# Optimization experiments

Hardware: AMD Instinct MI355X
Metric: run time of the kernel (lower is better)

The kernel has to match this reference:

```python
import jax, jax.numpy as jnp
import numpy as np

DX, DY, MR, MBAR, NT, B, GOUT = 16, 8, 64, 256, 9, 4, 64
HX, EX, HRNN, HB = 1024, 512, 512, 2048
BB_IN = 1 + EX + HRNN


def setup_inputs() -> dict:
    key = jax.random.key(0)
    ks = jax.random.split(key, 12)
    total = (NT - 1) * MBAR + 1  # 2049 hidden-process time points
    X = jax.random.randint(ks[0], (B, total, DX), 0, 50).astype(jnp.float32)  # molecule counts
    Y = jax.random.normal(ks[1], (B, NT, DY), dtype=jnp.float32)
    # R: cumulative integrated reaction rates (non-decreasing in time)
    R = jnp.cumsum(jax.random.uniform(ks[2], (B, total, MR), dtype=jnp.float32) * 0.01, axis=1)
    stoich = (jax.random.randint(ks[3], (DX, MR), 0, 3) - 1).astype(jnp.float32)  # entries in {-1,0,1}
    times_t = jnp.linspace(0.0, 8.0, NT).astype(jnp.float32)
    times_tau = jnp.linspace(0.0, 1.0, MBAR).astype(jnp.float32)
    sc = lambda k, sh: jax.random.normal(k, sh, dtype=jnp.float32) * np.float32(1.0 / np.sqrt(sh[0]))
    Wx1, bx1 = sc(ks[4], (DX, HX)), jnp.zeros(HX, jnp.float32)
    Wx2, bx2 = sc(ks[5], (HX, EX)), jnp.zeros(EX, jnp.float32)
    Wih = sc(ks[6], (DY, HRNN))
    Whh = sc(ks[7], (HRNN, HRNN))
    bh = jnp.zeros(HRNN, jnp.float32)
    Wb1, bb1 = sc(ks[8], (BB_IN, HB)), jnp.zeros(HB, jnp.float32)
    Wb2, bb2 = sc(ks[9], (HB, GOUT)), jnp.zeros(GOUT, jnp.float32)
    return dict(X=X, Y=Y, R=R, stoich=stoich, times_t=times_t, times_tau=times_tau,
                Wx1=Wx1, bx1=bx1, Wx2=Wx2, bx2=bx2, Wih=Wih, Whh=Whh, bh=bh,
                Wb1=Wb1, bb1=bb1, Wb2=Wb2, bb2=bb2, k=1, k_prime=1, q=0, q_prime=1)


def reference(X, Y, R, stoich, times_t, times_tau,
              Wx1, bx1, Wx2, bx2, Wih, Whh, bh, Wb1, bb1, Wb2, bb2,
              k, k_prime, q, q_prime):
    """stochastic_integral_vectorized: gather displaced states, run the
    martingale network forward on base and displaced states, masked
    accumulation weighted by rate increments. Returns [GOUT]."""
    m_bar = times_tau.shape[0]
    base = k_prime * m_bar

    # --- Y encoder (Elman RNN over the observation slice, final hidden state) ---
    Yslice = Y[q, k + 1:, :]                       # [T_rem, DY]
    def rnn_step(h, y):
        return jnp.tanh(y @ Wih + h @ Whh + bh), None
    eY, _ = jax.lax.scan(rnn_step, jnp.zeros(Whh.shape[0], X.dtype), Yslice)  # [HRNN]

    # --- batched martingale forward: t [N], Xb [N, DX] -> [N, GOUT] ---
    def batched_forward(t, Xb):
        eX = jnp.tanh(Xb @ Wx1 + bx1) @ Wx2 + bx2          # [N, EX]
        eYb = jnp.broadcast_to(eY, (Xb.shape[0], eY.shape[0]))
        inp = jnp.concatenate([t[:, None], eX, eYb], axis=1)  # [N, 1+EX+HRNN]
        return jnp.tanh(inp @ Wb1 + bb1) @ Wb2 + bb2       # [N, GOUT]

    Xbase = X[q_prime, base:base + m_bar, :]               # [M_bar, DX]
    t = times_t[k] + times_tau                              # [M_bar]
    nn = batched_forward(t, Xbase)                          # [M_bar, GOUT]

    mr = stoich.shape[1]
    X_disp = Xbase[None, :, :] + stoich.T[:, None, :]       # [MR, M_bar, DX]
    valid = jnp.all(X_disp >= 0, axis=-1)                   # [MR, M_bar]
    nn_disp = batched_forward(jnp.tile(t, mr),
                              X_disp.reshape(mr * m_bar, -1)).reshape(mr, m_bar, -1)

    R_delta = R[q_prime, base + 1:base + m_bar + 1, :] - R[q_prime, base:base + m_bar, :]  # [M_bar, MR]
    si = jnp.einsum('jmg,mj,jm->g', nn_disp - nn[None], R_delta, valid.astype(nn.dtype))
    return si
```

## Files before the change

kernel.cpp:

```cpp
#include <hip/hip_runtime.h>
#include <math.h>

#define DXc   16
#define MRc   64
#define MBARc 256
#define NTc   9
#define DYc   8
#define HXc   1024
#define EXc   512
#define HRc   512
#define HBc   2048
#define GOUTc 64
#define TOTc  2049

using bf16x8 = __attribute__((ext_vector_type(8))) short;
using f32x4  = __attribute__((ext_vector_type(4))) float;

typedef unsigned int u32;
typedef u32 __attribute__((address_space(1))) gbl_u32;
typedef u32 __attribute__((address_space(3))) lds_u32;

__device__ __forceinline__ float fast_tanh(float x){
    float e = __expf(2.0f * x);
    return 1.0f - 2.0f / (e + 1.0f);
}

__device__ __forceinline__ short f2bf(float f){
    unsigned u = __builtin_bit_cast(unsigned, f);
    u = (u + 0x7FFFu + ((u >> 16) & 1u)) >> 16;
    return (short)u;
}

__device__ __forceinline__ void gld_lds16(const short* g, short* l){
    __builtin_amdgcn_global_load_lds((const gbl_u32*)g, (lds_u32*)l, 16, 0, 0);
}

__global__ void prep_kernel(const float* __restrict__ stoich, const float* __restrict__ Wx1,
                            const float* __restrict__ Wx2, const float* __restrict__ Wb1,
                            const float* __restrict__ X, const float* __restrict__ R,
                            const float* __restrict__ bx1, const float* __restrict__ bx2,
                            const int* kpptr, const int* qpptr,
                            float* __restrict__ SW, short* __restrict__ Wx2a,
                            short* __restrict__ Wb1p, float* __restrict__ XW,
                            float* __restrict__ T1, float* __restrict__ wrow,
                            float* __restrict__ hb0, float* __restrict__ dacc,
                            float* __restrict__ outz, float* __restrict__ eXb,
                            int* __restrict__ cnt){
    int b = blockIdx.x, tid = threadIdx.x;
    if (b < 256){
        int idx = b * 256 + tid;
        int j = idx >> 10, c = idx & 1023;
        float acc = 0.f;
        #pragma unroll
        for (int d = 0; d < DXc; ++d) acc += stoich[d * MRc + j] * Wx1[d * HXc + c];
        SW[idx] = acc;
    } else if (b < 512){
        size_t grp = (size_t)(b - 256) * 256 + tid;
        int lane = grp & 63;
        size_t t2 = grp >> 6;
        int kt = t2 & 15, mt = t2 >> 4;
        int c  = mt * 16 + (lane & 15);
        int e0 = kt * 32 + ((lane >> 4) << 3);
        short o8[8];
        #pragma unroll
        for (int jj = 0; jj < 8; ++jj) o8[jj] = f2bf(Wx2[(size_t)c * EXc + e0 + jj]);
        *(bf16x8*)(Wx2a + grp * 8) = *(bf16x8*)o8;
    } else if (b < 1024){
        size_t grp = (size_t)(b - 512) * 256 + tid;
        int lane = grp & 63;
        size_t t2 = grp >> 6;
        int kt = t2 & 15, nt = t2 >> 4;
        int n  = nt * 16 + (lane & 15);
        int k0 = kt * 32 + ((lane >> 4) << 3);
        short o8[8];
        #pragma unroll
        for (int jj = 0; jj < 8; ++jj) o8[jj] = f2bf(Wb1[(size_t)(1 + k0 + jj) * HBc + n]);
        *(bf16x8*)(Wb1p + grp * 8) = *(bf16x8*)o8;
    } else if (b < 2048){
        int idx = (b - 1024) * 256 + tid;
        int m = idx >> 10, c = idx & 1023;
        int base = kpptr[0] * MBARc;
        const float* xr = X + ((size_t)qpptr[0] * TOTc + base + m) * DXc;
        float acc = bx1[c];
        #pragma unroll
        for (int d = 0; d < DXc; ++d) acc += xr[d] * Wx1[d * HXc + c];
        XW[idx] = acc;
        T1[idx] = fast_tanh(acc);
    } else if (b < 2112){
        int j = b - 2048, m = tid;
        int base = kpptr[0] * MBARc;
        int qp = qpptr[0];
        const float* xr = X + ((size_t)qp * TOTc + base + m) * DXc;
        bool valid = true;
        #pragma unroll
        for (int d = 0; d < DXc; ++d) valid = valid && (xr[d] + stoich[d * MRc + j] >= 0.f);
        size_t rb = (size_t)qp * TOTc * MRc;
        float rd = R[rb + (size_t)(base + 1 + m) * MRc + j] - R[rb + (size_t)(base + m) * MRc + j];
        wrow[j * MBARc + m] = valid ? rd : 0.f;
    } else if (b == 2112){
        hb0[tid] = 0.f; hb0[tid + 256] = 0.f;
        #pragma unroll
        for (int l = 0; l < 8; ++l) dacc[tid + l * 256] = 0.f;
        if (tid < GOUTc) outz[tid] = 0.f;
        if (tid < 4) cnt[tid] = 0;
    } else {
        int idx = (b - 2113) * 256 + tid;
        eXb[idx] = bx2[idx & 511];
    }
}

#define MMGRID(aa, bb) {                                                       \
    _Pragma("unroll") for (int i_ = 0; i_ < 4; ++i_)                           \
        _Pragma("unroll") for (int j_ = 0; j_ < 4; ++j_)                       \
            acc[i_][j_] = __builtin_amdgcn_mfma_f32_16x16x32_bf16(aa[i_], bb[j_], acc[i_][j_], 0, 0, 0); }

__device__ __forceinline__ void stage32(const short* __restrict__ Ap, const short* __restrict__ Bp,
                                        short* As, short* Bs,
                                        int at0, int bt0, int s, int KTOT, int wave, int lane){
    #pragma unroll
    for (int c = 0; c < 4; ++c){
        int ci = wave * 4 + c;
        int half = ci >> 3;
        int t    = ci & 7;
        const short* src = half ? (Bp + ((size_t)(bt0 + t) * KTOT + s) * 512 + lane * 8)
                                : (Ap + ((size_t)(at0 + t) * KTOT + s) * 512 + lane * 8);
        short* dst = (half ? Bs : As) + t * 512;
        gld_lds16(src, dst);
    }
}

#define STAGE_COMPUTE(As, Bs) {                                                       \
    bf16x8 af[4], bfr[4];                                                             \
    _Pragma("unroll") for (int i_ = 0; i_ < 4; ++i_)                                  \
        af[i_] = *(const bf16x8*)((As) + ((wm * 4 + i_) * 512) + lane * 8);           \
    _Pragma("unroll") for (int j_ = 0; j_ < 4; ++j_)                                  \
        bfr[j_] = *(const bf16x8*)((Bs) + ((wn * 4 + j_) * 512) + lane * 8);          \
    MMGRID(af, bfr); }

__global__ __launch_bounds__(256) void mega2_kernel(
    const float* __restrict__ Y, const float* __restrict__ Wih,
    const float* __restrict__ Whh, const float* __restrict__ bh,
    const float* __restrict__ Wb1, const float* __restrict__ bb1,
    const int* kptr, const int* qptr,
    float* __restrict__ hb0, float* __restrict__ hb1,
    int* __restrict__ cnt, float* __restrict__ cY,
    const short* __restrict__ Wx2a, const short* __restrict__ Wb1p,
    short* __restrict__ W12p,
    const float* __restrict__ Wx2, float* __restrict__ eXb,
    float* __restrict__ Z2Bacc,
    const float* __restrict__ XW, const float* __restrict__ T1,
    const float* __restrict__ SW, short* __restrict__ A1p){
    __shared__ __align__(16) char smem[34816];
    int b = blockIdx.x, tid = threadIdx.x;
    if (b < 8){
        float* hs   = (float*)smem;
        float (*psum)[64] = (float(*)[64])(smem + 2048);
        int o = tid & 63, seg = tid >> 6;
        int out = b * 64 + o;
        int k = kptr[0], q = qptr[0];
        hs[tid] = 0.f; hs[tid + 256] = 0.f;
        __syncthreads();
        for (int s = 0; s < 8; ++s){
            float* dst = (s & 1) ? hb0 : hb1;
            if (s > 0){
                const float* src = (s & 1) ? hb1 : hb0;
                if (tid == 0){
                    int guard = 0;
                    while (__hip_atomic_load(cnt, __ATOMIC_ACQUIRE, __HIP_MEMORY_SCOPE_AGENT) < 8 * s
                           && ++guard < (1 << 26)) {}
                }
                __syncthreads();
                hs[tid]       = __hip_atomic_load(src + tid,       __ATOMIC_RELAXED, __HIP_MEMORY_SCOPE_AGENT);
                hs[tid + 256] = __hip_atomic_load(src + tid + 256, __ATOMIC_RELAXED, __HIP_MEMORY_SCOPE_AGENT);
                __syncthreads();
            }
            int t = k + 1 + s;
            if (t < NTc){
                int k0 = seg * 128;
                float a0 = 0.f, a1 = 0.f, a2 = 0.f, a3 = 0.f;
                #pragma unroll 4
                for (int kk = 0; kk < 128; kk += 4){
                    a0 += hs[k0 + kk + 0] * Whh[(size_t)(k0 + kk + 0) * HRc + out];
                    a1 += hs[k0 + kk + 1] * Whh[(size_t)(k0 + kk + 1) * HRc + out];
                    a2 += hs[k0 + kk + 2] * Whh[(size_t)(k0 + kk + 2) * HRc + out];
                    a3 += hs[k0 + kk + 3] * Whh[(size_t)(k0 + kk + 3) * HRc + out];
                }
                psum[seg][o] = (a0 + a1) + (a2 + a3);
                __syncthreads();
                if (seg == 0){
                    float a = psum[0][o] + psum[1][o] + psum[2][o] + psum[3][o];
                    const float* y = Y + (q * NTc + t) * DYc;
                    float z = bh[out];
                    #pragma unroll
                    for (int d = 0; d < DYc; ++d) z += y[d] * Wih[d * HRc + out];
                    __hip_atomic_store(dst + out, fast_tanh(z + a), __ATOMIC_RELEASE, __HIP_MEMORY_SCOPE_AGENT);
                }
                __syncthreads();
            } else {
                if (seg == 0)
                    __hip_atomic_store(dst + out, hs[out], __ATOMIC_RELEASE, __HIP_MEMORY_SCOPE_AGENT);
                __syncthreads();
            }
            if (tid == 0)
                __hip_atomic_fetch_add(cnt, 1, __ATOMIC_RELEASE, __HIP_MEMORY_SCOPE_AGENT);
        }
        if (tid == 0){
            int guard = 0;
            while (__hip_atomic_load(cnt, __ATOMIC_ACQUIRE, __HIP_MEMORY_SCOPE_AGENT) < 64
                   && ++guard < (1 << 26)) {}
        }
        __syncthreads();
        hs[tid]       = __hip_atomic_load(hb0 + tid,       __ATOMIC_RELAXED, __HIP_MEMORY_SCOPE_AGENT);
        hs[tid + 256] = __hip_atomic_load(hb0 + tid + 256, __ATOMIC_RELAXED, __HIP_MEMORY_SCOPE_AGENT);
        __syncthreads();
        int h = b * 256 + tid;
        float acc = 0.f;
        #pragma unroll 4
        for (int e = 0; e < HRc; ++e)
            acc += hs[e] * Wb1[(size_t)(1 + EXc + e) * HBc + h];
        cY[h] = bb1[h] + acc;
    } else if (b < 136){
        short* As0 = (short*)smem;
        short* As1 = (short*)(smem + 8192);
        short* Bs0 = (short*)(smem + 16384);
        short* Bs1 = (short*)(smem + 24576);
        const int KTOT = 16, S = 16;
        int wave = tid >> 6, lane = tid & 63;
        int wm = wave >> 1, wn = wave & 1;
        int b2 = b - 8;
        int bx = b2 & 15, by = b2 >> 4;
        int quad = lane >> 4, llo = lane & 15;
        f32x4 acc[4][4];
        #pragma unroll
        for (int i = 0; i < 4; ++i)
            #pragma unroll
            for (int j = 0; j < 4; ++j) acc[i][j] = (f32x4){0.f, 0.f, 0.f, 0.f};
        stage32(Wx2a, Wb1p, As0, Bs0, by * 8, bx * 8, 0, KTOT, wave, lane);
        for (int s = 0; s < S; ++s){
            short* Asc = (s & 1) ? As1 : As0;
            short* Bsc = (s & 1) ? Bs1 : Bs0;
            short* Asn = (s & 1) ? As0 : As1;
            short* Bsn = (s & 1) ? Bs0 : Bs1;
            __syncthreads();
            if (s + 1 < S)
                stage32(Wx2a, Wb1p, Asn, Bsn, by * 8, bx * 8, s + 1, KTOT, wave, lane);
            STAGE_COMPUTE(Asc, Bsc);
        }
        #pragma unroll
        for (int j = 0; j < 4; ++j){
            int h = bx * 128 + wn * 64 + j * 16 + llo;
            #pragma unroll
            for (int i = 0; i < 4; ++i){
                #pragma unroll
                for (int r = 0; r < 4; ++r){
                    int c = by * 128 + wm * 64 + i * 16 + quad * 4 + r;
                    W12p[(((size_t)(h >> 4) * 32 + (c >> 5)) * 64 + ((c & 31) >> 3) * 16 + llo) * 8 + (c & 7)] =
                        f2bf(acc[i][j][r]);
                }
            }
        }
    } else if (b < 648){
        float* t1s = (float*)smem;
        int bb = b - 136;
        int mg = bb & 31, eh = (bb >> 5) & 1, kq = bb >> 6;
        int m0 = mg * 8, e = eh * 256 + tid, k0 = kq * 128;
        #pragma unroll
        for (int l = 0; l < 4; ++l){
            int idx = tid + l * 256;
            t1s[idx] = T1[(size_t)(m0 + (idx >> 7)) * HXc + k0 + (idx & 127)];
        }
        __syncthreads();
        float acc[8] = {};
        #pragma unroll 4
        for (int kk = 0; kk < 128; ++kk){
            float wv = Wx2[(size_t)(k0 + kk) * EXc + e];
            #pragma unroll
            for (int mm = 0; mm < 8; ++mm) acc[mm] += t1s[mm * 128 + kk] * wv;
        }
        #pragma unroll
        for (int mm = 0; mm < 8; ++mm)
            atomicAdd(&eXb[(size_t)(m0 + mm) * EXc + e], acc[mm]);
        __syncthreads();
        if (tid == 0)
            __hip_atomic_fetch_add(cnt + 1, 1, __ATOMIC_RELEASE, __HIP_MEMORY_SCOPE_AGENT);
    } else if (b < 8840){
        size_t grp = (size_t)(b - 648) * 256 + tid;
        int lane = grp & 63;
        size_t t2 = grp >> 6;
        int kt = t2 & 31;
        int mt = (int)(t2 >> 5);
        int m  = mt * 16 + (lane & 15);
        int c0 = kt * 32 + ((lane >> 4) << 3);
        int j    = m >> 8;
        int mloc = m & 255;
        const float* xwr = XW + (size_t)mloc * HXc + c0;
        const float* t1r = T1 + (size_t)mloc * HXc + c0;
        const float* swr = SW + (size_t)j * HXc + c0;
        short o8[8];
        #pragma unroll
        for (int i = 0; i < 8; ++i)
            o8[i] = f2bf(fast_tanh(xwr[i] + swr[i]) - t1r[i]);
        *(bf16x8*)(A1p + grp * 8) = *(bf16x8*)o8;
    } else {
        float* exs = (float*)smem;
        if (tid == 0){
            int guard = 0;
            while (__hip_atomic_load(cnt + 1, __ATOMIC_ACQUIRE, __HIP_MEMORY_SCOPE_AGENT) < 512
                   && ++guard < (1 << 26)) {}
        }
        __syncthreads();
        int bb = b - 8840;
        int mg = bb & 31, hh = (bb >> 5) & 7, kq = bb >> 8;
        int m0 = mg * 8, h = hh * 256 + tid, k0 = kq * 256;
        #pragma unroll
        for (int l = 0; l < 8; ++l){
            int idx = tid + l * 256;
            exs[idx] = __hip_atomic_load(eXb + (size_t)(m0 + (idx >> 8)) * EXc + k0 + (idx & 255),
                                         __ATOMIC_RELAXED, __HIP_MEMORY_SCOPE_AGENT);
        }
        __syncthreads();
        float acc[8] = {};
        #pragma unroll 4
        for (int kk = 0; kk < 256; ++kk){
            float wv = Wb1[(size_t)(1 + k0 + kk) * HBc + h];
            #pragma unroll
            for (int mm = 0; mm < 8; ++mm) acc[mm] += exs[mm * 256 + kk] * wv;
        }
        #pragma unroll
        for (int mm = 0; mm < 8; ++mm)
            atomicAdd(&Z2Bacc[(size_t)(m0 + mm) * HBc + h], acc[mm]);
    }
}

__device__ __forceinline__ void stage24(const short* __restrict__ Ap, const short* __restrict__ Bp,
                                        short* As, short* Bs,
                                        int at0, int bt0, int s, int wave, int lane){
    #pragma unroll
    for (int c = 0; c < 6; ++c){
        int ci = wave * 6 + c;
        const short* src;
        short* dst;
        if (ci < 8){
            src = Ap + ((size_t)(at0 + ci) * 32 + s) * 512 + lane * 8;
            dst = As + ci * 512;
        } else {
            int t = ci - 8;
            src = Bp + ((size_t)(bt0 + t) * 32 + s) * 512 + lane * 8;
            dst = Bs + t * 512;
        }
        gld_lds16(src, dst);
    }
}

__global__ __launch_bounds__(256, 2) void gemm_big(
    const short* __restrict__ Ap, const short* __restrict__ Bp,
    const float* __restrict__ Z2Bacc, const float* __restrict__ Wb1,
    const float* __restrict__ cY, const float* __restrict__ times_t,
    const float* __restrict__ times_tau, const int* kptr,
    const float* __restrict__ wrow, float* __restrict__ dacc){
    const int S = 32;
    __shared__ __align__(16) short Asb[2][4096];
    __shared__ __align__(16) short Bsb[2][8192];
    int tid = threadIdx.x;
    int wave = tid >> 6, lane = tid & 63;
    int wm = wave >> 1, wn = wave & 1;
    int bm = blockIdx.x, bn = blockIdx.y;
    int quad = lane >> 4, llo = lane & 15;
    f32x4 acc[4][8];
    #pragma unroll
    for (int i = 0; i < 4; ++i)
        #pragma unroll
        for (int j = 0; j < 8; ++j) acc[i][j] = (f32x4){0.f, 0.f, 0.f, 0.f};
    stage24(Ap, Bp, Asb[0], Bsb[0], bm * 8, bn * 16, 0, wave, lane);
    for (int s = 0; s < S; ++s){
        int buf = s & 1;
        __syncthreads();
        if (s + 1 < S)
            stage24(Ap, Bp, Asb[buf ^ 1], Bsb[buf ^ 1], bm * 8, bn * 16, s + 1, wave, lane);
        {
            bf16x8 af[4], bfr[8];
            #pragma unroll
            for (int i = 0; i < 4; ++i)
                af[i] = *(const bf16x8*)(Asb[buf] + ((wm * 4 + i) * 512) + lane * 8);
            #pragma unroll
            for (int j = 0; j < 8; ++j)
                bfr[j] = *(const bf16x8*)(Bsb[buf] + ((wn * 8 + j) * 512) + lane * 8);
            #pragma unroll
            for (int i = 0; i < 4; ++i)
                #pragma unroll
                for (int j = 0; j < 8; ++j)
                    acc[i][j] = __builtin_amdgcn_mfma_f32_16x16x32_bf16(af[i], bfr[j], acc[i][j], 0, 0, 0);
        }
    }
    float tk = times_t[kptr[0]];
    int nj[8];
    float w0n[8], cyn[8];
    #pragma unroll
    for (int j = 0; j < 8; ++j){
        nj[j]  = bn * 256 + wn * 128 + j * 16 + llo;
        w0n[j] = Wb1[nj[j]];
        cyn[j] = cY[nj[j]];
    }
    float part[8] = {};
    #pragma unroll
    for (int i = 0; i < 4; ++i){
        #pragma unroll
        for (int r = 0; r < 4; ++r){
            int m = bm * 128 + wm * 64 + i * 16 + quad * 4 + r;
            float wr = wrow[m];
            float tm = tk + times_tau[m & 255];
            const float* zrow = Z2Bacc + (size_t)(m & 255) * HBc;
            #pragma unroll
            for (int j = 0; j < 8; ++j){
                float zb  = zrow[nj[j]] + tm * w0n[j] + cyn[j];
                float tb  = fast_tanh(zb);
                float tdz = fast_tanh(acc[i][j][r]);
                float num = tdz * (1.0f - tb * tb);
                float den = 1.0f + tb * tdz;
                part[j] += wr * num * __builtin_amdgcn_rcpf(den);
            }
        }
    }
    #pragma unroll
    for (int j = 0; j < 8; ++j){
        part[j] += __shfl_xor(part[j], 16);
        part[j] += __shfl_xor(part[j], 32);
    }
    __shared__ float redn[256];
    redn[tid] = 0.f;
    __syncthreads();
    if (lane < 16){
        #pragma unroll
        for (int j = 0; j < 8; ++j)
            atomicAdd(&redn[wn * 128 + j * 16 + llo], part[j]);
    }
    __syncthreads();
    atomicAdd(&dacc[bn * 256 + tid], redn[tid]);
}

__global__ void out_kernel(const float* __restrict__ dacc, const float* __restrict__ Wb2,
                           float* __restrict__ out){
    __shared__ float red[4][64];
    int tid = threadIdx.x;
    int g = tid & 63, seg = tid >> 6;
    int h0 = blockIdx.x * 256 + seg * 64;
    float s = 0.f;
    #pragma unroll 8
    for (int hh = 0; hh < 64; ++hh)
        s += dacc[h0 + hh] * Wb2[(size_t)(h0 + hh) * GOUTc + g];
    red[seg][g] = s;
    __syncthreads();
    if (tid < 64)
        atomicAdd(&out[tid], red[0][tid] + red[1][tid] + red[2][tid] + red[3][tid]);
}

extern "C" void kernel_launch(void* const* d_in, const int* in_sizes, int n_in,
                              void* d_out, int out_size, void* d_ws, size_t ws_size,
                              hipStream_t stream){
    const float* X         = (const float*)d_in[0];
    const float* Y         = (const float*)d_in[1];
    const float* R         = (const float*)d_in[2];
    const float* stoich    = (const float*)d_in[3];
    const float* times_t   = (const float*)d_in[4];
    const float* times_tau = (const float*)d_in[5];
    const float* Wx1 = (const float*)d_in[6];
    const float* bx1 = (const float*)d_in[7];
    const float* Wx2 = (const float*)d_in[8];
    const float* bx2 = (const float*)d_in[9];
    const float* Wih = (const float*)d_in[10];
    const float* Whh = (const float*)d_in[11];
    const float* bh  = (const float*)d_in[12];
    const float* Wb1 = (const float*)d_in[13];
    const float* bb1 = (const float*)d_in[14];
    const float* Wb2 = (const float*)d_in[15];
    const int* kp  = (const int*)d_in[17];
    const int* kpp = (const int*)d_in[18];
    const int* qp  = (const int*)d_in[19];
    const int* qpp = (const int*)d_in[20];
    float* out = (float*)d_out;

    float* ws     = (float*)d_ws;
    float* hb0    = ws;
    float* hb1    = ws + 512;
    float* cY     = ws + 1024;
    float* dacc   = ws + 3072;
    float* wrow   = ws + 5120;
    float* SW     = ws + 21504;
    float* XW     = ws + 87040;
    float* T1     = ws + 349184;
    float* eXb    = ws + 611328;
    float* Z2Bacc = ws + 742400;
    short* A1p    = (short*)(ws + 1266688);
    short* Wx2a   = (short*)(ws + 9655296);
    short* Wb1p   = (short*)(ws + 9917440);
    short* W12p   = (short*)(ws + 10441728);
    int*   cnt    = (int*)(ws + 11490304);

    hipMemsetAsync(Z2Bacc, 0, (size_t)MBARc * HBc * sizeof(float), stream);
    prep_kernel  <<<2625, 256, 0, stream>>>(stoich, Wx1, Wx2, Wb1, X, R, bx1, bx2, kpp, qpp,
                                            SW, Wx2a, Wb1p, XW, T1, wrow, hb0, dacc, out,
                                            eXb, cnt);
    mega2_kernel <<<9352, 256, 0, stream>>>(Y, Wih, Whh, bh, Wb1, bb1, kp, qp, hb0, hb1, cnt, cY,
                                            Wx2a, Wb1p, W12p, Wx2, eXb, Z2Bacc, XW, T1, SW, A1p);
    gemm_big     <<<dim3(128, 8), 256, 0, stream>>>(A1p, W12p, Z2Bacc, Wb1, cY,
                                                    times_t, times_tau, kp, wrow, dacc);
    out_kernel   <<<8,    256, 0, stream>>>(dacc, Wb2, out);
}
```

Baseline: 307.3 us.

## Move RNN encoder into final GEMM kernel and tile Wb1 repack via LDS

New measurement: 789.6 us. +157.0%, slower.

```diff
diff --git a/kernel.cpp b/kernel.cpp
--- a/kernel.cpp
+++ b/kernel.cpp
@@ -35,27 +35,54 @@
     __builtin_amdgcn_global_load_lds((const gbl_u32*)g, (lds_u32*)l, 16, 0, 0);
 }
 
-__global__ void prep_kernel(const float* __restrict__ stoich, const float* __restrict__ Wx1,
-                            const float* __restrict__ Wx2, const float* __restrict__ Wb1,
-                            const float* __restrict__ X, const float* __restrict__ R,
-                            const float* __restrict__ bx1, const float* __restrict__ bx2,
-                            const int* kpptr, const int* qpptr,
-                            float* __restrict__ SW, short* __restrict__ Wx2a,
-                            short* __restrict__ Wb1p, float* __restrict__ XW,
-                            float* __restrict__ T1, float* __restrict__ wrow,
-                            float* __restrict__ hb0, float* __restrict__ dacc,
-                            float* __restrict__ outz, float* __restrict__ eXb,
-                            int* __restrict__ cnt){
+__global__ __launch_bounds__(256) void prep_kernel(
+    const float* __restrict__ stoich, const float* __restrict__ Wx1,
+    const float* __restrict__ Wx2, const float* __restrict__ Wb1,
+    const float* __restrict__ X, const float* __restrict__ R,
+    const float* __restrict__ bx1, const float* __restrict__ bx2,
+    const int* kpptr, const int* qpptr,
+    float* __restrict__ SW, short* __restrict__ Wx2a,
+    short* __restrict__ Wb1p, float* __restrict__ XW,
+    float* __restrict__ T1, float* __restrict__ wrow,
+    float* __restrict__ dacc, float* __restrict__ outz,
+    float* __restrict__ eXb, int* __restrict__ cnt){
+    __shared__ __align__(16) short wtile[32 * 514];
     int b = blockIdx.x, tid = threadIdx.x;
-    if (b < 256){
-        int idx = b * 256 + tid;
+    if (b < 16){
+        int kt = b;
+        int krow0 = 1 + kt * 32;
+        for (int chunk = 0; chunk < 4; ++chunk){
+            int c0 = chunk * 512;
+            #pragma unroll
+            for (int l = 0; l < 64; ++l){
+                int idx = tid + l * 256;
+                int r = idx >> 9, c = idx & 511;
+                wtile[r * 514 + c] = f2bf(Wb1[(size_t)(krow0 + r) * HBc + c0 + c]);
+            }
+            __syncthreads();
+            #pragma unroll
+            for (int v = 0; v < 8; ++v){
+                int vecid = tid + v * 256;
+                int ntl = vecid >> 6, lane = vecid & 63;
+                int nl = ntl * 16 + (lane & 15);
+                int kl = (lane >> 4) * 8;
+                short o8[8];
+                #pragma unroll
+                for (int jj = 0; jj < 8; ++jj) o8[jj] = wtile[(kl + jj) * 514 + nl];
+                int nt = chunk * 32 + ntl;
+                *(bf16x8*)(Wb1p + (((size_t)nt * 16 + kt) * 64 + lane) * 8) = *(bf16x8*)o8;
+            }
+            __syncthreads();
+        }
+    } else if (b < 272){
+        int idx = (b - 16) * 256 + tid;
         int j = idx >> 10, c = idx & 1023;
         float acc = 0.f;
         #pragma unroll
         for (int d = 0; d < DXc; ++d) acc += stoich[d * MRc + j] * Wx1[d * HXc + c];
         SW[idx] = acc;
-    } else if (b < 512){
-        size_t grp = (size_t)(b - 256) * 256 + tid;
+    } else if (b < 528){
+        size_t grp = (size_t)(b - 272) * 256 + tid;
         int lane = grp & 63;
         size_t t2 = grp >> 6;
         int kt = t2 & 15, mt = t2 >> 4;
@@ -65,19 +92,8 @@
         #pragma unroll
         for (int jj = 0; jj < 8; ++jj) o8[jj] = f2bf(Wx2[(size_t)c * EXc + e0 + jj]);
         *(bf16x8*)(Wx2a + grp * 8) = *(bf16x8*)o8;
-    } else if (b < 1024){
-        size_t grp = (size_t)(b - 512) * 256 + tid;
-        int lane = grp & 63;
-        size_t t2 = grp >> 6;
-        int kt = t2 & 15, nt = t2 >> 4;
-        int n  = nt * 16 + (lane & 15);
-        int k0 = kt * 32 + ((lane >> 4) << 3);
-        short o8[8];
-        #pragma unroll
-        for (int jj = 0; jj < 8; ++jj) o8[jj] = f2bf(Wb1[(size_t)(1 + k0 + jj) * HBc + n]);
-        *(bf16x8*)(Wb1p + grp * 8) = *(bf16x8*)o8;
-    } else if (b < 2048){
-        int idx = (b - 1024) * 256 + tid;
+    } else if (b < 1552){
+        int idx = (b - 528) * 256 + tid;
         int m = idx >> 10, c = idx & 1023;
         int base = kpptr[0] * MBARc;
         const float* xr = X + ((size_t)qpptr[0] * TOTc + base + m) * DXc;
@@ -86,8 +102,8 @@
         for (int d = 0; d < DXc; ++d) acc += xr[d] * Wx1[d * HXc + c];
         XW[idx] = acc;
         T1[idx] = fast_tanh(acc);
-    } else if (b < 2112){
-        int j = b - 2048, m = tid;
+    } else if (b < 1616){
+        int j = b - 1552, m = tid;
         int base = kpptr[0] * MBARc;
         int qp = qpptr[0];
         const float* xr = X + ((size_t)qp * TOTc + base + m) * DXc;
@@ -97,14 +113,13 @@
         size_t rb = (size_t)qp * TOTc * MRc;
         float rd = R[rb + (size_t)(base + 1 + m) * MRc + j] - R[rb + (size_t)(base + m) * MRc + j];
         wrow[j * MBARc + m] = valid ? rd : 0.f;
-    } else if (b == 2112){
-        hb0[tid] = 0.f; hb0[tid + 256] = 0.f;
+    } else if (b == 1616){
         #pragma unroll
         for (int l = 0; l < 8; ++l) dacc[tid + l * 256] = 0.f;
         if (tid < GOUTc) outz[tid] = 0.f;
         if (tid < 4) cnt[tid] = 0;
     } else {
-        int idx = (b - 2113) * 256 + tid;
+        int idx = (b - 1617) * 256 + tid;
         eXb[idx] = bx2[idx & 511];
     }
 }
@@ -137,24 +152,167 @@
         bfr[j_] = *(const bf16x8*)((Bs) + ((wn * 4 + j_) * 512) + lane * 8);          \
     MMGRID(af, bfr); }
 
-__global__ __launch_bounds__(256) void mega2_kernel(
-    const float* __restrict__ Y, const float* __restrict__ Wih,
-    const float* __restrict__ Whh, const float* __restrict__ bh,
-    const float* __restrict__ Wb1, const float* __restrict__ bb1,
-    const int* kptr, const int* qptr,
-    float* __restrict__ hb0, float* __restrict__ hb1,
-    int* __restrict__ cnt, float* __restrict__ cY,
+__global__ __launch_bounds__(256) void mega_kernel(
     const short* __restrict__ Wx2a, const short* __restrict__ Wb1p,
     short* __restrict__ W12p,
     const float* __restrict__ Wx2, float* __restrict__ eXb,
-    float* __restrict__ Z2Bacc,
+    const float* __restrict__ Wb1, float* __restrict__ Z2Bacc,
     const float* __restrict__ XW, const float* __restrict__ T1,
-    const float* __restrict__ SW, short* __restrict__ A1p){
-    __shared__ __align__(16) char smem[34816];
+    const float* __restrict__ SW, short* __restrict__ A1p,
+    int* __restrict__ cnt){
+    __shared__ __align__(16) char smem[32768];
     int b = blockIdx.x, tid = threadIdx.x;
+    if (b < 128){
+        short* As0 = (short*)smem;
+        short* As1 = (short*)(smem + 8192);
+        short* Bs0 = (short*)(smem + 16384);
+        short* Bs1 = (short*)(smem + 24576);
+        const int KTOT = 16, S = 16;
+        int wave = tid >> 6, lane = tid & 63;
+        int wm = wave >> 1, wn = wave & 1;
+        int bx = b & 15, by = b >> 4;
+        int quad = lane >> 4, llo = lane & 15;
+        f32x4 acc[4][4];
+        #pragma unroll
+        for (int i = 0; i < 4; ++i)
+            #pragma unroll
+            for (int j = 0; j < 4; ++j) acc[i][j] = (f32x4){0.f, 0.f, 0.f, 0.f};
+        stage32(Wx2a, Wb1p, As0, Bs0, by * 8, bx * 8, 0, KTOT, wave, lane);
+        for (int s = 0; s < S; ++s){
+            short* Asc = (s & 1) ? As1 : As0;
+            short* Bsc = (s & 1) ? Bs1 : Bs0;
+            short* Asn = (s & 1) ? As0 : As1;
+            short* Bsn = (s & 1) ? Bs0 : Bs1;
+            __syncthreads();
+            if (s + 1 < S)
+                stage32(Wx2a, Wb1p, Asn, Bsn, by * 8, bx * 8, s + 1, KTOT, wave, lane);
+            STAGE_COMPUTE(Asc, Bsc);
+        }
+        #pragma unroll
+        for (int j = 0; j < 4; ++j){
+            int h = bx * 128 + wn * 64 + j * 16 + llo;
+            #pragma unroll
+            for (int i = 0; i < 4; ++i){
+                #pragma unroll
+                for (int r = 0; r < 4; ++r){
+                    int c = by * 128 + wm * 64 + i * 16 + quad * 4 + r;
+                    W12p[(((size_t)(h >> 4) * 32 + (c >> 5)) * 64 + ((c & 31) >> 3) * 16 + llo) * 8 + (c & 7)] =
+                        f2bf(acc[i][j][r]);
+                }
+            }
+        }
+    } else if (b < 640){
+        float* t1s = (float*)smem;
+        int bb = b - 128;
+        int mg = bb & 31, eh = (bb >> 5) & 1, kq = bb >> 6;
+        int m0 = mg * 8, e = eh * 256 + tid, k0 = kq * 128;
+        #pragma unroll
+        for (int l = 0; l < 4; ++l){
+            int idx = tid + l * 256;
+            t1s[idx] = T1[(size_t)(m0 + (idx >> 7)) * HXc + k0 + (idx & 127)];
+        }
+        __syncthreads();
+        float acc[8] = {};
+        #pragma unroll 4
+        for (int kk = 0; kk < 128; ++kk){
+            float wv = Wx2[(size_t)(k0 + kk) * EXc + e];
+            #pragma unroll
+            for (int mm = 0; mm < 8; ++mm) acc[mm] += t1s[mm * 128 + kk] * wv;
+        }
+        #pragma unroll
+        for (int mm = 0; mm < 8; ++mm)
+            atomicAdd(&eXb[(size_t)(m0 + mm) * EXc + e], acc[mm]);
+        __syncthreads();
+        if (tid == 0)
+            __hip_atomic_fetch_add(cnt + 1, 1, __ATOMIC_RELEASE, __HIP_MEMORY_SCOPE_AGENT);
+    } else if (b < 8832){
+        size_t grp = (size_t)(b - 640) * 256 + tid;
+        int lane = grp & 63;
+        size_t t2 = grp >> 6;
+        int kt = t2 & 31;
+        int mt = (int)(t2 >> 5);
+        int m  = mt * 16 + (lane & 15);
+        int c0 = kt * 32 + ((lane >> 4) << 3);
+        int j    = m >> 8;
+        int mloc = m & 255;
+        const float* xwr = XW + (size_t)mloc * HXc + c0;
+        const float* t1r = T1 + (size_t)mloc * HXc + c0;
+        const float* swr = SW + (size_t)j * HXc + c0;
+        short o8[8];
+        #pragma unroll
+        for (int i = 0; i < 8; ++i)
+            o8[i] = f2bf(fast_tanh(xwr[i] + swr[i]) - t1r[i]);
+        *(bf16x8*)(A1p + grp * 8) = *(bf16x8*)o8;
+    } else {
+        float* exs = (float*)smem;
+        if (tid == 0){
+            int guard = 0;
+            while (__hip_atomic_load(cnt + 1, __ATOMIC_ACQUIRE, __HIP_MEMORY_SCOPE_AGENT) < 512
+                   && ++guard < (1 << 26)) {}
+        }
+        __syncthreads();
+        int bb = b - 8832;
+        int mg = bb & 31, hh = (bb >> 5) & 7, kq = bb >> 8;
+        int m0 = mg * 8, h = hh * 256 + tid, k0 = kq * 256;
+        #pragma unroll
+        for (int l = 0; l < 8; ++l){
+            int idx = tid + l * 256;
+            exs[idx] = __hip_atomic_load(eXb + (size_t)(m0 + (idx >> 8)) * EXc + k0 + (idx & 255),
+                                         __ATOMIC_RELAXED, __HIP_MEMORY_SCOPE_AGENT);
+        }
+        __syncthreads();
+        float acc[8] = {};
+        #pragma unroll 4
+        for (int kk = 0; kk < 256; ++kk){
+            float wv = Wb1[(size_t)(1 + k0 + kk) * HBc + h];
+            #pragma unroll
+            for (int mm = 0; mm < 8; ++mm) acc[mm] += exs[mm * 256 + kk] * wv;
+        }
+        #pragma unroll
+        for (int mm = 0; mm < 8; ++mm)
+            atomicAdd(&Z2Bacc[(size_t)(m0 + mm) * HBc + h], acc[mm]);
+    }
+}
+
+__device__ __forceinline__ void stage24(const short* __restrict__ Ap, const short* __restrict__ Bp,
+                                        short* As, short* Bs,
+                                        int at0, int bt0, int s, int wave, int lane){
+    #pragma unroll
+    for (int c = 0; c < 6; ++c){
+        int ci = wave * 6 + c;
+        const short* src;
+        short* dst;
+        if (ci < 8){
+            src = Ap + ((size_t)(at0 + ci) * 32 + s) * 512 + lane * 8;
+            dst = As + ci * 512;
+        } else {
+            int t = ci - 8;
+            src = Bp + ((size_t)(bt0 + t) * 32 + s) * 512 + lane * 8;
+            dst = Bs + t * 512;
+        }
+        gld_lds16(src, dst);
+    }
+}
+
+__global__ __launch_bounds__(256, 2) void gemm_rnn(
+    const short* __restrict__ Ap, const short* __restrict__ Bp,
+    const float* __restrict__ Z2Bacc, const float* __restrict__ Wb1,
+    const float* __restrict__ bb1, float* __restrict__ cY,
+    const float* __restrict__ times_t, const float* __restrict__ times_tau,
+    const int* kptr, const int* qptr,
+    const float* __restrict__ Y, const float* __restrict__ Wih,
+    const float* __restrict__ Whh, const float* __restrict__ bh,
+    float* __restrict__ hb0, float* __restrict__ hb1, int* __restrict__ cnt,
+    const float* __restrict__ wrow, float* __restrict__ dacc){
+    const int S = 32;
+    __shared__ __align__(16) short Asb[2][4096];
+    __shared__ __align__(16) short Bsb[2][8192];
+    __shared__ float redn[256];
+    int tid = threadIdx.x;
+    int b = blockIdx.x;
     if (b < 8){
-        float* hs   = (float*)smem;
-        float (*psum)[64] = (float(*)[64])(smem + 2048);
+        float* hs = (float*)&Asb[0][0];
+        float (*psum)[64] = (float(*)[64])&Bsb[0][0];
         int o = tid & 63, seg = tid >> 6;
         int out = b * 64 + o;
         int k = kptr[0], q = qptr[0];
@@ -218,153 +376,16 @@
         #pragma unroll 4
         for (int e = 0; e < HRc; ++e)
             acc += hs[e] * Wb1[(size_t)(1 + EXc + e) * HBc + h];
-        cY[h] = bb1[h] + acc;
-    } else if (b < 136){
-        short* As0 = (short*)smem;
-        short* As1 = (short*)(smem + 8192);
-        short* Bs0 = (short*)(smem + 16384);
-        short* Bs1 = (short*)(smem + 24576);
-        const int KTOT = 16, S = 16;
-        int wave = tid >> 6, lane = tid & 63;
-        int wm = wave >> 1, wn = wave & 1;
-        int b2 = b - 8;
-        int bx = b2 & 15, by = b2 >> 4;
-        int quad = lane >> 4, llo = lane & 15;
-        f32x4 acc[4][4];
-        #pragma unroll
-        for (int i = 0; i < 4; ++i)
-            #pragma unroll
-            for (int j = 0; j < 4; ++j) acc[i][j] = (f32x4){0.f, 0.f, 0.f, 0.f};
-        stage32(Wx2a, Wb1p, As0, Bs0, by * 8, bx * 8, 0, KTOT, wave, lane);
-        for (int s = 0; s < S; ++s){
-            short* Asc = (s & 1) ? As1 : As0;
-            short* Bsc = (s & 1) ? Bs1 : Bs0;
-            short* Asn = (s & 1) ? As0 : As1;
-            short* Bsn = (s & 1) ? Bs0 : Bs1;
-            __syncthreads();
-            if (s + 1 < S)
-                stage32(Wx2a, Wb1p, Asn, Bsn, by * 8, bx * 8, s + 1, KTOT, wave, lane);
-            STAGE_COMPUTE(Asc, Bsc);
-        }
-        #pragma unroll
-        for (int j = 0; j < 4; ++j){
-            int h = bx * 128 + wn * 64 + j * 16 + llo;
-            #pragma unroll
-            for (int i = 0; i < 4; ++i){
-                #pragma unroll
-                for (int r = 0; r < 4; ++r){
-                    int c = by * 128 + wm * 64 + i * 16 + quad * 4 + r;
-                    W12p[(((size_t)(h >> 4) * 32 + (c >> 5)) * 64 + ((c & 31) >> 3) * 16 + llo) * 8 + (c & 7)] =
-                        f2bf(acc[i][j][r]);
-                }
-            }
-        }
-    } else if (b < 648){
-        float* t1s = (float*)smem;
-        int bb = b - 136;
-        int mg = bb & 31, eh = (bb >> 5) & 1, kq = bb >> 6;
-        int m0 = mg * 8, e = eh * 256 + tid, k0 = kq * 128;
-        #pragma unroll
-        for (int l = 0; l < 4; ++l){
-            int idx = tid + l * 256;
-            t1s[idx] = T1[(size_t)(m0 + (idx >> 7)) * HXc + k0 + (idx & 127)];
-        }
-        __syncthreads();
-        float acc[8] = {};
-        #pragma unroll 4
-        for (int kk = 0; kk < 128; ++kk){
-            float wv = Wx2[(size_t)(k0 + kk) * EXc + e];
-            #pragma unroll
-            for (int mm = 0; mm < 8; ++mm) acc[mm] += t1s[mm * 128 + kk] * wv;
-        }
-        #pragma unroll
-        for (int mm = 0; mm < 8; ++mm)
-            atomicAdd(&eXb[(size_t)(m0 + mm) * EXc + e], acc[mm]);
+        __hip_atomic_store(cY + h, bb1[h] + acc, __ATOMIC_RELEASE, __HIP_MEMORY_SCOPE_AGENT);
         __syncthreads();
         if (tid == 0)
-            __hip_atomic_fetch_add(cnt + 1, 1, __ATOMIC_RELEASE, __HIP_MEMORY_SCOPE_AGENT);
-    } else if (b < 8840){
-        size_t grp = (size_t)(b - 648) * 256 + tid;
-        int lane = grp & 63;
-        size_t t2 = grp >> 6;
-        int kt = t2 & 31;
-        int mt = (int)(t2 >> 5);
-        int m  = mt * 16 + (lane & 15);
-        int c0 = kt * 32 + ((lane >> 4) << 3);
-        int j    = m >> 8;
-        int mloc = m & 255;
-        const float* xwr = XW + (size_t)mloc * HXc + c0;
-        const float* t1r = T1 + (size_t)mloc * HXc + c0;
-        const float* swr = SW + (size_t)j * HXc + c0;
-        short o8[8];
-        #pragma unroll
-        for (int i = 0; i < 8; ++i)
-            o8[i] = f2bf(fast_tanh(xwr[i] + swr[i]) - t1r[i]);
-        *(bf16x8*)(A1p + grp * 8) = *(bf16x8*)o8;
-    } else {
-        float* exs = (float*)smem;
-        if (tid == 0){
-            int guard = 0;
-            while (__hip_atomic_load(cnt + 1, __ATOMIC_ACQUIRE, __HIP_MEMORY_SCOPE_AGENT) < 512
-                   && ++guard < (1 << 26)) {}
-        }
-        __syncthreads();
-        int bb = b - 8840;
-        int mg = bb & 31, hh = (bb >> 5) & 7, kq = bb >> 8;
-        int m0 = mg * 8, h = hh * 256 + tid, k0 = kq * 256;
-        #pragma unroll
-        for (int l = 0; l < 8; ++l){
-            int idx = tid + l * 256;
-            exs[idx] = __hip_atomic_load(eXb + (size_t)(m0 + (idx >> 8)) * EXc + k0 + (idx & 255),
-                                         __ATOMIC_RELAXED, __HIP_MEMORY_SCOPE_AGENT);
-        }
-        __syncthreads();
-        float acc[8] = {};
-        #pragma unroll 4
-        for (int kk = 0; kk < 256; ++kk){
-            float wv = Wb1[(size_t)(1 + k0 + kk) * HBc + h];
-            #pragma unroll
-            for (int mm = 0; mm < 8; ++mm) acc[mm] += exs[mm * 256 + kk] * wv;
-        }
-        #pragma unroll
-        for (int mm = 0; mm < 8; ++mm)
-            atomicAdd(&Z2Bacc[(size_t)(m0 + mm) * HBc + h], acc[mm]);
-    }
-}
-
-__device__ __forceinline__ void stage24(const short* __restrict__ Ap, const short* __restrict__ Bp,
-                                        short* As, short* Bs,
-                                        int at0, int bt0, int s, int wave, int lane){
-    #pragma unroll
-    for (int c = 0; c < 6; ++c){
-        int ci = wave * 6 + c;
-        const short* src;
-        short* dst;
-        if (ci < 8){
-            src = Ap + ((size_t)(at0 + ci) * 32 + s) * 512 + lane * 8;
-            dst = As + ci * 512;
-        } else {
-            int t = ci - 8;
-            src = Bp + ((size_t)(bt0 + t) * 32 + s) * 512 + lane * 8;
-            dst = Bs + t * 512;
-        }
-        gld_lds16(src, dst);
-    }
-}
-
-__global__ __launch_bounds__(256, 2) void gemm_big(
-    const short* __restrict__ Ap, const short* __restrict__ Bp,
-    const float* __restrict__ Z2Bacc, const float* __restrict__ Wb1,
-    const float* __restrict__ cY, const float* __restrict__ times_t,
-    const float* __restrict__ times_tau, const int* kptr,
-    const float* __restrict__ wrow, float* __restrict__ dacc){
-    const int S = 32;
-    __shared__ __align__(16) short Asb[2][4096];
-    __shared__ __align__(16) short Bsb[2][8192];
-    int tid = threadIdx.x;
+            __hip_atomic_fetch_add(cnt + 2, 1, __ATOMIC_RELEASE, __HIP_MEMORY_SCOPE_AGENT);
+        return;
+    }
+    int bg = b - 8;
+    int bm = bg & 127, bn = bg >> 7;
     int wave = tid >> 6, lane = tid & 63;
     int wm = wave >> 1, wn = wave & 1;
-    int bm = blockIdx.x, bn = blockIdx.y;
     int quad = lane >> 4, llo = lane & 15;
     f32x4 acc[4][8];
     #pragma unroll
@@ -392,6 +413,12 @@
                     acc[i][j] = __builtin_amdgcn_mfma_f32_16x16x32_bf16(af[i], bfr[j], acc[i][j], 0, 0, 0);
         }
     }
+    if (tid == 0){
+        int guard = 0;
+        while (__hip_atomic_load(cnt + 2, __ATOMIC_ACQUIRE, __HIP_MEMORY_SCOPE_AGENT) < 8
+               && ++guard < (1 << 26)) {}
+    }
+    __syncthreads();
     float tk = times_t[kptr[0]];
     int nj[8];
     float w0n[8], cyn[8];
@@ -399,7 +426,7 @@
     for (int j = 0; j < 8; ++j){
         nj[j]  = bn * 256 + wn * 128 + j * 16 + llo;
         w0n[j] = Wb1[nj[j]];
-        cyn[j] = cY[nj[j]];
+        cyn[j] = __hip_atomic_load(cY + nj[j], __ATOMIC_RELAXED, __HIP_MEMORY_SCOPE_AGENT);
     }
     float part[8] = {};
     #pragma unroll
@@ -426,7 +453,6 @@
         part[j] += __shfl_xor(part[j], 16);
         part[j] += __shfl_xor(part[j], 32);
     }
-    __shared__ float redn[256];
     redn[tid] = 0.f;
     __syncthreads();
     if (lane < 16){
@@ -497,12 +523,12 @@
     int*   cnt    = (int*)(ws + 11490304);
 
     hipMemsetAsync(Z2Bacc, 0, (size_t)MBARc * HBc * sizeof(float), stream);
-    prep_kernel  <<<2625, 256, 0, stream>>>(stoich, Wx1, Wx2, Wb1, X, R, bx1, bx2, kpp, qpp,
-                                            SW, Wx2a, Wb1p, XW, T1, wrow, hb0, dacc, out,
-                                            eXb, cnt);
-    mega2_kernel <<<9352, 256, 0, stream>>>(Y, Wih, Whh, bh, Wb1, bb1, kp, qp, hb0, hb1, cnt, cY,
-                                            Wx2a, Wb1p, W12p, Wx2, eXb, Z2Bacc, XW, T1, SW, A1p);
-    gemm_big     <<<dim3(128, 8), 256, 0, stream>>>(A1p, W12p, Z2Bacc, Wb1, cY,
-                                                    times_t, times_tau, kp, wrow, dacc);
-    out_kernel   <<<8,    256, 0, stream>>>(dacc, Wb2, out);
-}
+    prep_kernel <<<2129, 256, 0, stream>>>(stoich, Wx1, Wx2, Wb1, X, R, bx1, bx2, kpp, qpp,
+                                           SW, Wx2a, Wb1p, XW, T1, wrow, dacc, out, eXb, cnt);
+    mega_kernel <<<9344, 256, 0, stream>>>(Wx2a, Wb1p, W12p, Wx2, eXb, Wb1, Z2Bacc,
+                                           XW, T1, SW, A1p, cnt);
+    gemm_rnn    <<<1032, 256, 0, stream>>>(A1p, W12p, Z2Bacc, Wb1, bb1, cY,
+                                           times_t, times_tau, kp, qp,
+                                           Y, Wih, Whh, bh, hb0, hb1, cnt, wrow, dacc);
+    out_kernel  <<<8,    256, 0, stream>>>(dacc, Wb2, out);
+}
```
